# Kernel tuning notes

Measured on AMD Instinct MI355X. Metric: run time of the kernel, lower is better.

Reference implementation:

```python
import jax, jax.numpy as jnp
import numpy as np

# --- dims derived from init_kwargs ---
K = 16                 # top-k patches
NUM_SAMPLES = 500      # MC samples for perturbed top-k
SIGMA = 0.05
PATCH = 128            # patch_size
H_SCORE, W_SCORE = 16, 16
SCALE_H, SCALE_W = 64, 64          # high // score
# padding per DPS.__init__: padded = scale*score + patch - 1
TOP_PAD = (PATCH - SCALE_H) // 2    # 32
LEFT_PAD = (PATCH - SCALE_W) // 2   # 32
BOTTOM_PAD = (SCALE_H * H_SCORE + PATCH - 1) - TOP_PAD - 1024   # 95
RIGHT_PAD = (SCALE_W * W_SCORE + PATCH - 1) - LEFT_PAD - 1024   # 95


def setup_inputs() -> dict:
    key = jax.random.key(0)
    k1, k2 = jax.random.split(key)
    x_high = jax.random.normal(k1, (8, 3, 1024, 1024), dtype=jnp.float32)
    scores_2d = jax.random.uniform(k2, (8, H_SCORE, W_SCORE), dtype=jnp.float32)
    return {"x_high": x_high, "scores_2d": scores_2d}


def _perturbed_topk_indicators(scores):
    # scores: (b, d) ; faithful to PerturbedTopKFunction.forward
    b, d = scores.shape
    noise = jax.random.normal(jax.random.key(42), (b, NUM_SAMPLES, d), dtype=scores.dtype)
    perturbed = scores[:, None, :] + noise * SIGMA          # (b, n, d)
    idx = jax.lax.top_k(perturbed, K)[1]                    # (b, n, k)
    idx = jnp.sort(idx, axis=-1)                            # torch sorts indices ascending
    onehot = jax.nn.one_hot(idx, d, dtype=scores.dtype)     # (b, n, k, d)
    return onehot.mean(axis=1)                              # (b, k, d)


def _dps_forward(x_high, scores_2d, indicators_fn):
    b, c = x_high.shape[:2]
    # min-max normalize scores
    s = scores_2d.reshape(b, -1)
    smin = s.min(axis=-1, keepdims=True)
    smax = s.max(axis=-1, keepdims=True)
    s = (s - smin) / (smax - smin + 1e-5)
    ind = indicators_fn(s).reshape(b, K, H_SCORE, W_SCORE)  # soft top-k indicators

    x_pad = jnp.pad(x_high, ((0, 0), (0, 0), (TOP_PAD, BOTTOM_PAD), (LEFT_PAD, RIGHT_PAD)))
    # column window indices for all w_score grid cells: (W_SCORE, PATCH)
    col_idx = (jnp.arange(W_SCORE) * SCALE_W)[:, None] + jnp.arange(PATCH)[None, :]

    def row_step(acc, i):
        # rows of all patches in grid-row i: (b, c, PATCH, W_pad)
        row = jax.lax.dynamic_slice_in_dim(x_pad, i * SCALE_H, PATCH, axis=2)
        wins = row[:, :, :, col_idx]                        # (b, c, PATCH, W_SCORE, PATCH)
        w = jax.lax.dynamic_slice_in_dim(ind, i, 1, axis=2)[:, :, 0, :]  # (b, k, W_SCORE)
        acc = acc + jnp.einsum('bcpwq,bkw->bkcpq', wins, w)
        return acc, None

    patches0 = jnp.zeros((b, K, c, PATCH, PATCH), dtype=x_high.dtype)
    patches, _ = jax.lax.scan(row_step, patches0, jnp.arange(H_SCORE))
    return patches.reshape(-1, c, PATCH, PATCH)


def reference(x_high, scores_2d):
    return _dps_forward(x_high, scores_2d, _perturbed_topk_indicators)
```

## Files before the change

kernel.cpp:

```cpp
#include <hip/hip_runtime.h>
#include <stdint.h>


#define NSAMP 500
#define DDIM  256

__device__ __forceinline__ void threefry2x32_0_42(uint32_t x0, uint32_t x1,
                                                  uint32_t& o0, uint32_t& o1) {
  const uint32_t k0 = 0u, k1 = 42u;
  const uint32_t k2 = k0 ^ k1 ^ 0x1BD11BDAu;
  x0 += k0; x1 += k1;
#define TF_ROUND(r) { x0 += x1; x1 = (x1 << (r)) | (x1 >> (32 - (r))); x1 ^= x0; }
  TF_ROUND(13) TF_ROUND(15) TF_ROUND(26) TF_ROUND(6)
  x0 += k1; x1 += k2 + 1u;
  TF_ROUND(17) TF_ROUND(29) TF_ROUND(16) TF_ROUND(24)
  x0 += k2; x1 += k0 + 2u;
  TF_ROUND(13) TF_ROUND(15) TF_ROUND(26) TF_ROUND(6)
  x0 += k0; x1 += k1 + 3u;
  TF_ROUND(17) TF_ROUND(29) TF_ROUND(16) TF_ROUND(24)
  x0 += k1; x1 += k2 + 4u;
  TF_ROUND(13) TF_ROUND(15) TF_ROUND(26) TF_ROUND(6)
  x0 += k2; x1 += k0 + 5u;
#undef TF_ROUND
  o0 = x0; o1 = x1;
}

__device__ __forceinline__ float xla_erfinv(float x) {
#pragma clang fp contract(off)
  float w = -log1pf(-x * x);
  float p;
  if (w < 5.0f) {
    w = w - 2.5f;
    p = 2.81022636e-08f;
    p = 3.43273939e-07f + p * w;
    p = -3.5233877e-06f + p * w;
    p = -4.39150654e-06f + p * w;
    p = 0.00021858087f + p * w;
    p = -0.00125372503f + p * w;
    p = -0.00417768164f + p * w;
    p = 0.246640727f + p * w;
    p = 1.50140941f + p * w;
  } else {
    w = sqrtf(w) - 3.0f;
    p = -0.000200214257f;
    p = 0.000100950558f + p * w;
    p = 0.00134934322f + p * w;
    p = -0.00367342844f + p * w;
    p = 0.00573950773f + p * w;
    p = -0.0076224613f + p * w;
    p = 0.00943887047f + p * w;
    p = 1.00167406f + p * w;
    p = 2.83297682f + p * w;
  }
  return p * x;
}

__global__ void __launch_bounds__(256) topk_kernel(const float* __restrict__ scores,
                                                   uint32_t* __restrict__ counts) {
#pragma clang fp contract(off)
  const int gs = blockIdx.x;
  const int b = gs / NSAMP;
  const int n = gs - b * NSAMP;
  const int d = threadIdx.x;
  const int lane = d & 63, wv = d >> 6;

  __shared__ float pvs[DDIM];
  __shared__ float wmx[4], wmn[4];
  __shared__ int wtot[4];

  const float sc = scores[b * DDIM + d];

  float mx = sc, mn = sc;
  for (int off = 32; off > 0; off >>= 1) {
    mx = fmaxf(mx, __shfl_xor(mx, off));
    mn = fminf(mn, __shfl_xor(mn, off));
  }
  if (lane == 0) { wmx[wv] = mx; wmn[wv] = mn; }
  __syncthreads();
  mx = fmaxf(fmaxf(wmx[0], wmx[1]), fmaxf(wmx[2], wmx[3]));
  mn = fminf(fminf(wmn[0], wmn[1]), fminf(wmn[2], wmn[3]));
  const float denom = (mx - mn) + 1e-5f;

  const uint32_t j = (uint32_t)(b * (NSAMP * DDIM) + n * DDIM + d);
  uint32_t o0, o1;
  threefry2x32_0_42(0u, j, o0, o1);
  const uint32_t bits = o0 ^ o1;
  const float flo = -0.99999994f;
  float f = __uint_as_float((bits >> 9) | 0x3f800000u) - 1.0f;
  float u = f * 2.0f + flo;
  u = fmaxf(flo, u);
  const float z = 1.41421356237f * xla_erfinv(u);
  const float sv = (sc - mn) / denom;
  const float pv = sv + z * 0.05f;

  pvs[d] = pv;
  __syncthreads();

  const float4* pv4 = (const float4*)pvs;
  int gc = 0, eqb = 0;
  for (int e4 = 0; e4 < DDIM / 4; ++e4) {
    float4 o = pv4[e4];
    int e = e4 << 2;
    gc += (o.x > pv); gc += (o.y > pv); gc += (o.z > pv); gc += (o.w > pv);
    eqb += (o.x == pv) & ((e + 0) < d);
    eqb += (o.y == pv) & ((e + 1) < d);
    eqb += (o.z == pv) & ((e + 2) < d);
    eqb += (o.w == pv) & ((e + 3) < d);
  }
  const bool sel = (gc + eqb) < 16;

  const unsigned long long m = __ballot(sel);
  if (lane == 0) wtot[wv] = __popcll(m);
  __syncthreads();
  int r = __popcll(m & ((1ull << lane) - 1ull));
  for (int w2 = 0; w2 < wv; ++w2) r += wtot[w2];

  if (sel) atomicAdd(&counts[(b << 12) + (r << 8) + d], 1u);
}

__global__ void __launch_bounds__(256) patches_kernel(const float* __restrict__ x,
                                                      const uint32_t* __restrict__ counts,
                                                      float* __restrict__ out) {
  const int p0 = blockIdx.x << 3;
  const int c  = blockIdx.y;
  const int zb = blockIdx.z;
  const int b  = zb >> 1;
  const int k0 = (zb & 1) << 3;

  __shared__ __align__(16) float cw[DDIM * 8];
  __shared__ int colOff[DDIM];
  __shared__ int wcnt[4];

  const int tid = threadIdx.x;
  const int lane = tid & 63, wvi = tid >> 6;

  {
    float wreg[8];
    bool any = false;
#pragma unroll
    for (int kk = 0; kk < 8; ++kk) {
      float w = (float)counts[((b * 16 + k0 + kk) << 8) + tid] / 500.0f;
      wreg[kk] = w;
      any = any || (w != 0.0f);
    }
    unsigned long long m = __ballot(any);
    if (lane == 0) wcnt[wvi] = __popcll(m);
    __syncthreads();
    int base = 0;
    for (int w2 = 0; w2 < wvi; ++w2) base += wcnt[w2];
    if (any) {
      int pos = base + __popcll(m & ((1ull << lane) - 1ull));
      colOff[pos] = ((tid >> 4) << 16) | ((tid & 15) << 6);
#pragma unroll
      for (int kk = 0; kk < 8; ++kk) cw[pos * 8 + kk] = wreg[kk];
    }
    __syncthreads();
  }
  const int nact = wcnt[0] + wcnt[1] + wcnt[2] + wcnt[3];

  const int q0   = (tid & 31) << 2;
  const int slot = tid >> 5;
  const int ps   = p0 + slot;

  int qm = 0xFFFF, ym = 0xFFFF;
  if (q0 < 32) qm &= ~1;
  if (q0 > 92) qm &= ~0x8000;
  if (ps < 32) ym &= ~1;
  if (ps > 95) ym &= ~0x8000;
  const int baseOff = (ps - 32) * 1024 + q0 - 32;

  float4 acc[8];
#pragma unroll
  for (int kk = 0; kk < 8; ++kk) acc[kk] = make_float4(0.f, 0.f, 0.f, 0.f);

  const float* xim = x + ((size_t)(b * 3 + c) << 20);

  float4 xv = make_float4(0.f, 0.f, 0.f, 0.f);
  int okc = 0;
  if (nact > 0) {
    const int co = colOff[0];
    okc = (qm >> ((co >> 6) & 15)) & (ym >> (co >> 16)) & 1;
    xv = *(const float4*)(xim + (okc ? (baseOff + co) : 0));
  }

  for (int it = 0; it < nact; ++it) {
    const int itn = (it + 1 < nact) ? it + 1 : it;
    const int con = colOff[itn];
    const int okn = (qm >> ((con >> 6) & 15)) & (ym >> (con >> 16)) & 1;
    const float4 xn = *(const float4*)(xim + (okn ? (baseOff + con) : 0));

    float4 xc = xv;
    xc.x = okc ? xc.x : 0.0f;
    xc.y = okc ? xc.y : 0.0f;
    xc.z = okc ? xc.z : 0.0f;
    xc.w = okc ? xc.w : 0.0f;

    const float4 wa = *(const float4*)&cw[it * 8 + 0];
    const float4 wb = *(const float4*)&cw[it * 8 + 4];

#define ACC_K(kk, wv_)                                            \
    { acc[kk].x += (wv_) * xc.x; acc[kk].y += (wv_) * xc.y;       \
      acc[kk].z += (wv_) * xc.z; acc[kk].w += (wv_) * xc.w; }
    ACC_K(0, wa.x) ACC_K(1, wa.y) ACC_K(2, wa.z) ACC_K(3, wa.w)
    ACC_K(4, wb.x) ACC_K(5, wb.y) ACC_K(6, wb.z) ACC_K(7, wb.w)
#undef ACC_K

    xv = xn;
    okc = okn;
  }

#pragma unroll
  for (int kk = 0; kk < 8; ++kk) {
    const size_t obase = ((size_t)((b * 16 + k0 + kk) * 3 + c)) << 14;
    float4* dst = (float4*)(out + obase + (size_t)ps * 128 + q0);
    __builtin_nontemporal_store(acc[kk].x, &dst->x);
    __builtin_nontemporal_store(acc[kk].y, &dst->y);
    __builtin_nontemporal_store(acc[kk].z, &dst->z);
    __builtin_nontemporal_store(acc[kk].w, &dst->w);
  }
}

extern "C" void kernel_launch(void* const* d_in, const int* in_sizes, int n_in,
                              void* d_out, int out_size, void* d_ws, size_t ws_size,
                              hipStream_t stream) {
  const float* x_high = (const float*)d_in[0];
  const float* scores = (const float*)d_in[1];
  float* out = (float*)d_out;
  uint32_t* counts = (uint32_t*)d_ws;

  hipMemsetAsync(counts, 0, 8 * 16 * DDIM * sizeof(uint32_t), stream);
  topk_kernel<<<8 * NSAMP, 256, 0, stream>>>(scores, counts);
  patches_kernel<<<dim3(16, 3, 16), 256, 0, stream>>>(x_high, counts, out);
}
```

Measured before the change: 197.1 us.

## Compute all 16 k-slots per patch block and use packed 64-bit keys for ranking

```diff
diff --git a/kernel.cpp b/kernel.cpp
--- a/kernel.cpp
+++ b/kernel.cpp
@@ -64,7 +64,7 @@
   const int d = threadIdx.x;
   const int lane = d & 63, wv = d >> 6;
 
-  __shared__ float pvs[DDIM];
+  __shared__ __align__(16) unsigned long long pk[DDIM];
   __shared__ float wmx[4], wmn[4];
   __shared__ int wtot[4];
 
@@ -93,21 +93,21 @@
   const float sv = (sc - mn) / denom;
   const float pv = sv + z * 0.05f;
 
-  pvs[d] = pv;
+  const uint32_t pu = __float_as_uint(pv);
+  const uint32_t mk = (pu & 0x80000000u) ? ~pu : (pu | 0x80000000u);
+  const unsigned long long key =
+      ((unsigned long long)mk << 32) | (unsigned long long)(255 - d);
+  pk[d] = key;
   __syncthreads();
 
-  const float4* pv4 = (const float4*)pvs;
-  int gc = 0, eqb = 0;
-  for (int e4 = 0; e4 < DDIM / 4; ++e4) {
-    float4 o = pv4[e4];
-    int e = e4 << 2;
-    gc += (o.x > pv); gc += (o.y > pv); gc += (o.z > pv); gc += (o.w > pv);
-    eqb += (o.x == pv) & ((e + 0) < d);
-    eqb += (o.y == pv) & ((e + 1) < d);
-    eqb += (o.z == pv) & ((e + 2) < d);
-    eqb += (o.w == pv) & ((e + 3) < d);
-  }
-  const bool sel = (gc + eqb) < 16;
+  int rank = 0;
+  const ulonglong2* pk2 = (const ulonglong2*)pk;
+  for (int e2 = 0; e2 < DDIM / 2; ++e2) {
+    ulonglong2 kk = pk2[e2];
+    rank += (kk.x > key);
+    rank += (kk.y > key);
+  }
+  const bool sel = rank < 16;
 
   const unsigned long long m = __ballot(sel);
   if (lane == 0) wtot[wv] = __popcll(m);
@@ -118,16 +118,14 @@
   if (sel) atomicAdd(&counts[(b << 12) + (r << 8) + d], 1u);
 }
 
-__global__ void __launch_bounds__(256) patches_kernel(const float* __restrict__ x,
-                                                      const uint32_t* __restrict__ counts,
-                                                      float* __restrict__ out) {
+__global__ void __launch_bounds__(256, 3) patches_kernel(const float* __restrict__ x,
+                                                         const uint32_t* __restrict__ counts,
+                                                         float* __restrict__ out) {
   const int p0 = blockIdx.x << 3;
   const int c  = blockIdx.y;
-  const int zb = blockIdx.z;
-  const int b  = zb >> 1;
-  const int k0 = (zb & 1) << 3;
-
-  __shared__ __align__(16) float cw[DDIM * 8];
+  const int b  = blockIdx.z;
+
+  __shared__ __align__(16) float cw[DDIM * 16];
   __shared__ int colOff[DDIM];
   __shared__ int wcnt[4];
 
@@ -135,11 +133,11 @@
   const int lane = tid & 63, wvi = tid >> 6;
 
   {
-    float wreg[8];
+    float wreg[16];
     bool any = false;
 #pragma unroll
-    for (int kk = 0; kk < 8; ++kk) {
-      float w = (float)counts[((b * 16 + k0 + kk) << 8) + tid] / 500.0f;
+    for (int kk = 0; kk < 16; ++kk) {
+      float w = (float)counts[(b << 12) + (kk << 8) + tid] / 500.0f;
       wreg[kk] = w;
       any = any || (w != 0.0f);
     }
@@ -152,7 +150,7 @@
       int pos = base + __popcll(m & ((1ull << lane) - 1ull));
       colOff[pos] = ((tid >> 4) << 16) | ((tid & 15) << 6);
 #pragma unroll
-      for (int kk = 0; kk < 8; ++kk) cw[pos * 8 + kk] = wreg[kk];
+      for (int kk = 0; kk < 16; ++kk) cw[pos * 16 + kk] = wreg[kk];
     }
     __syncthreads();
   }
@@ -169,9 +167,9 @@
   if (ps > 95) ym &= ~0x8000;
   const int baseOff = (ps - 32) * 1024 + q0 - 32;
 
-  float4 acc[8];
-#pragma unroll
-  for (int kk = 0; kk < 8; ++kk) acc[kk] = make_float4(0.f, 0.f, 0.f, 0.f);
+  float4 acc[16];
+#pragma unroll
+  for (int kk = 0; kk < 16; ++kk) acc[kk] = make_float4(0.f, 0.f, 0.f, 0.f);
 
   const float* xim = x + ((size_t)(b * 3 + c) << 20);
 
@@ -195,14 +193,18 @@
     xc.z = okc ? xc.z : 0.0f;
     xc.w = okc ? xc.w : 0.0f;
 
-    const float4 wa = *(const float4*)&cw[it * 8 + 0];
-    const float4 wb = *(const float4*)&cw[it * 8 + 4];
+    const float4 wa = *(const float4*)&cw[it * 16 + 0];
+    const float4 wb = *(const float4*)&cw[it * 16 + 4];
+    const float4 wc = *(const float4*)&cw[it * 16 + 8];
+    const float4 wd = *(const float4*)&cw[it * 16 + 12];
 
 #define ACC_K(kk, wv_)                                            \
     { acc[kk].x += (wv_) * xc.x; acc[kk].y += (wv_) * xc.y;       \
       acc[kk].z += (wv_) * xc.z; acc[kk].w += (wv_) * xc.w; }
-    ACC_K(0, wa.x) ACC_K(1, wa.y) ACC_K(2, wa.z) ACC_K(3, wa.w)
-    ACC_K(4, wb.x) ACC_K(5, wb.y) ACC_K(6, wb.z) ACC_K(7, wb.w)
+    ACC_K(0,  wa.x) ACC_K(1,  wa.y) ACC_K(2,  wa.z) ACC_K(3,  wa.w)
+    ACC_K(4,  wb.x) ACC_K(5,  wb.y) ACC_K(6,  wb.z) ACC_K(7,  wb.w)
+    ACC_K(8,  wc.x) ACC_K(9,  wc.y) ACC_K(10, wc.z) ACC_K(11, wc.w)
+    ACC_K(12, wd.x) ACC_K(13, wd.y) ACC_K(14, wd.z) ACC_K(15, wd.w)
 #undef ACC_K
 
     xv = xn;
@@ -210,8 +212,8 @@
   }
 
 #pragma unroll
-  for (int kk = 0; kk < 8; ++kk) {
-    const size_t obase = ((size_t)((b * 16 + k0 + kk) * 3 + c)) << 14;
+  for (int kk = 0; kk < 16; ++kk) {
+    const size_t obase = ((size_t)((b * 16 + kk) * 3 + c)) << 14;
     float4* dst = (float4*)(out + obase + (size_t)ps * 128 + q0);
     __builtin_nontemporal_store(acc[kk].x, &dst->x);
     __builtin_nontemporal_store(acc[kk].y, &dst->y);
@@ -230,5 +232,5 @@
 
   hipMemsetAsync(counts, 0, 8 * 16 * DDIM * sizeof(uint32_t), stream);
   topk_kernel<<<8 * NSAMP, 256, 0, stream>>>(scores, counts);
-  patches_kernel<<<dim3(16, 3, 16), 256, 0, stream>>>(x_high, counts, out);
-}
+  patches_kernel<<<dim3(16, 3, 8), 256, 0, stream>>>(x_high, counts, out);
+}
```

Result: slower. 202.0 us (+2.5%).
